# Optimization experiments

Hardware: AMD Instinct MI355X
Metric: run time of the kernel (lower is better)

## Reference

```python
import jax, jax.numpy as jnp
import numpy as np

B = 8192
N_SUP = 4
N_EXH = 4
N_OUTER = 50      # solver default; torch loop breaks early on tol/stall, replicated via done mask
N_INNER = 15
TOL = 1e-3
DESIGN_PRESSURE = 500.0
DESIGN_FLOW = 2.0
MAX_PRESSURE = 800.0
MOTOR_EFF = 0.9


def setup_inputs() -> dict:
    key = jax.random.key(0)
    k1, k2, k3 = jax.random.split(key, 3)
    fan_speed = 0.5 + 0.5 * jax.random.uniform(k1, (B,), dtype=jnp.float32)
    supply_damper_pos = 0.2 + 0.8 * jax.random.uniform(k2, (B, N_SUP), dtype=jnp.float32)
    exhaust_damper_pos = 0.2 + 0.8 * jax.random.uniform(k3, (B, N_EXH), dtype=jnp.float32)
    # FanModel.__init__ parameter init
    max_flow = DESIGN_FLOW * 1.3
    a_init = MAX_PRESSURE * 1000.0
    c_init = -MAX_PRESSURE * 1000.0 / max_flow ** 2
    b_init = (DESIGN_PRESSURE - a_init - c_init * DESIGN_FLOW ** 2) / DESIGN_FLOW
    fan_a = jnp.asarray(a_init / 1000.0, jnp.float32)
    fan_b = jnp.asarray(b_init, jnp.float32)
    fan_c = jnp.asarray(c_init, jnp.float32)
    # BranchModel / DamperModel parameter init (vectorized over branches)
    def branch_params(n):
        return (jnp.full((n,), np.log(50.0), jnp.float32),            # log_R_duct
                jnp.full((n,), 5.0, jnp.float32),                     # R_linear
                jnp.full((n,), np.log(10.0), jnp.float32),            # damper log_R_open
                jnp.full((n,), np.log(100000.0 / 10.0), jnp.float32)) # damper k
    slr, srl, sdo, sdk = branch_params(N_SUP)
    elr, erl, edo, edk = branch_params(N_EXH)
    return {
        'fan_speed': fan_speed,
        'supply_damper_pos': supply_damper_pos,
        'exhaust_damper_pos': exhaust_damper_pos,
        'fan_a': fan_a, 'fan_b': fan_b, 'fan_c': fan_c,
        'sup_log_R_duct': slr, 'sup_R_linear': srl, 'sup_damp_log_R_open': sdo, 'sup_damp_k': sdk,
        'exh_log_R_duct': elr, 'exh_R_linear': erl, 'exh_damp_log_R_open': edo, 'exh_damp_k': edk,
    }


def _branch_dp(flow, pos, log_R_duct, R_linear, damp_log_R_open, damp_k):
    # flow, pos: [B, n]; params: [n]; flow_exponent == 2.0
    aq = jnp.abs(flow)
    dp_duct = jnp.exp(log_R_duct) * aq ** 2 + jnp.abs(R_linear) * aq
    R_damp = jnp.exp(damp_log_R_open) * jnp.exp(damp_k * (1.0 - pos))
    return dp_duct + R_damp * aq ** 2


def _distribute(total_flow, pos, bp):
    n = pos.shape[1]
    flows = jnp.broadcast_to(total_flow[:, None] / n, pos.shape)
    for _ in range(N_INNER):
        p = _branch_dp(flows, pos, *bp)
        target = p.mean(axis=1, keepdims=True)
        R_eq = p / (flows ** 2 + 1e-6)
        new = jnp.sqrt(jnp.clip(target / (R_eq + 1e-6), 0.0, None))
        flows = new * total_flow[:, None] / (new.sum(axis=1, keepdims=True) + 1e-6)
    return flows, _branch_dp(flows, pos, *bp)


def _fan_pressure(flow, speed, a, b, c):
    fn = flow / (speed + 1e-6)
    pd = a * 1000.0 + b * fn + c * fn ** 2
    return jnp.maximum(pd * speed ** 2, 0.0)


def _forward(fan_speed, supply_damper_pos, exhaust_damper_pos, fan_a, fan_b, fan_c,
             sup_bp, exh_bp):
    def system_pressure(flow):
        _, sp = _distribute(flow, supply_damper_pos, sup_bp)
        _, ep = _distribute(flow, exhaust_damper_pos, exh_bp)
        return sp[:, 0] + ep[:, 0]

    flow_scale = DESIGN_FLOW / (DESIGN_PRESSURE + 1e-6)

    def step(carry, i):
        flow, prev_err, stall, done = carry
        res = _fan_pressure(flow, fan_speed, fan_a, fan_b, fan_c) - system_pressure(flow)
        err = jnp.max(jnp.abs(res))
        stalled = jnp.abs(err - prev_err) < 1e-6
        stall = jnp.where(stalled, stall + 1, 0)
        done = done | (err < TOL) | (stall > 10)
        alpha = jnp.maximum(0.5 * 0.95 ** i, 0.05)
        flow_new = jnp.clip(flow + alpha * res * flow_scale, 0.01, DESIGN_FLOW * 1.5)
        flow = jnp.where(done, flow, flow_new)
        prev_err = jnp.where(done, prev_err, err)
        return (flow, prev_err, stall, done), None

    init = (fan_speed * DESIGN_FLOW,
            jnp.asarray(jnp.inf, jnp.float32),
            jnp.asarray(0, jnp.int32),
            jnp.asarray(False))
    (flow, _, _, _), _ = jax.lax.scan(step, init, jnp.arange(N_OUTER, dtype=jnp.float32))

    flow = jnp.maximum(flow, 0.0)
    fan_p = _fan_pressure(flow, fan_speed, fan_a, fan_b, fan_c)
    sys_p = system_pressure(flow)
    # FanModel.get_power
    fr = flow / (DESIGN_FLOW + 1e-6)
    pr = fan_p / (DESIGN_PRESSURE + 1e-6)
    eta = jnp.clip(0.65 * (1.0 - 0.3 * (fr - 1.0) ** 2 - 0.2 * (pr - 1.0) ** 2), 0.3, 0.75)
    power = flow * fan_p / (eta * MOTOR_EFF + 1e-6)
    sf, sp = _distribute(flow, supply_damper_pos, sup_bp)
    ef, ep = _distribute(flow, exhaust_damper_pos, exh_bp)
    # pack dict outputs into one [B, 4 + 2*N_SUP + 2*N_EXH] array
    return jnp.concatenate([flow[:, None], fan_p[:, None], sys_p[:, None], power[:, None],
                            sf, sp, ef, ep], axis=1)


def reference(fan_speed, supply_damper_pos, exhaust_damper_pos, fan_a, fan_b, fan_c,
              sup_log_R_duct, sup_R_linear, sup_damp_log_R_open, sup_damp_k,
              exh_log_R_duct, exh_R_linear, exh_damp_log_R_open, exh_damp_k):
    sup_bp = (sup_log_R_duct, sup_R_linear, sup_damp_log_R_open, sup_damp_k)
    exh_bp = (exh_log_R_duct, exh_R_linear, exh_damp_log_R_open, exh_damp_k)
    return _forward(fan_speed, supply_damper_pos, exhaust_damper_pos,
                    fan_a, fan_b, fan_c, sup_bp, exh_bp)
```

## Files before the change

### kernel.cpp

```cpp
#include <hip/hip_runtime.h>
#include <math.h>

#define BATCH   8192
#define NOUTER  50
#define NINNER  15
#define NTHREADS (BATCH * 8)
#define NWAVES  (NTHREADS / 64)

__device__ __forceinline__ float fast_rcp(float x)  { return __builtin_amdgcn_rcpf(x); }
__device__ __forceinline__ float fast_sqrt(float x) { return __builtin_amdgcn_sqrtf(x); }

template <int CTRL>
__device__ __forceinline__ float dpp_movf(float x) {
    return __int_as_float(__builtin_amdgcn_update_dpp(
        0, __float_as_int(x), CTRL, 0xF, 0xF, true));
}
#define DPP_XOR1  0xB1
#define DPP_XOR2  0x4E
#define DPP_BQ0   0x00
#define DPP_ROR8  0x128
#define DPP_HMIR  0x141
#define DPP_BC15  0x142
#define DPP_BC31  0x143

__device__ __forceinline__ float distribute_lane(float total, float R2, float Rl,
                                                 float& pout) {
    float f = total * 0.25f;
#pragma unroll
    for (int it = 0; it < NINNER; ++it) {
        float p  = fmaf(R2, f * f, Rl * f);
        float t  = p + dpp_movf<DPP_XOR1>(p);
        t       += dpp_movf<DPP_XOR2>(t);
        float target = t * 0.25f;
        float q2e = fmaf(f, f, 1e-6f);
        float den = fmaf(q2e, 1e-6f, p);
        float ratio = target * q2e * fast_rcp(den);
        float nw = fast_sqrt(ratio);
        float s  = nw + dpp_movf<DPP_XOR1>(nw);
        s       += dpp_movf<DPP_XOR2>(s);
        f = nw * total * fast_rcp(s + 1e-6f);
    }
    pout = fmaf(R2, f * f, Rl * f);
    return f;
}

__device__ __forceinline__ float fan_pressure(float flow, float rspeed, float speed2,
                                              float a1000, float b, float c) {
    float fn = flow * rspeed;
    float pd = fmaf(c, fn * fn, fmaf(b, fn, a1000));
    return fmaxf(pd * speed2, 0.0f);
}

__device__ __forceinline__ float sys_from_p(float pfin) {
    float p0 = dpp_movf<DPP_BQ0>(pfin);
    return p0 + dpp_movf<DPP_HMIR>(p0);
}

struct LaneConsts {
    float R2, Rl;
    float speed, rspeed, speed2, a1000, b, c;
    int elem, lane, sub;
};

__device__ __forceinline__ LaneConsts setup_lane(
        const float* fan_speed,
        const float* sup_pos, const float* exh_pos,
        const float* pa, const float* pb, const float* pc,
        const float* slr, const float* srl, const float* sdo, const float* sdk,
        const float* elr, const float* erl, const float* edo, const float* edk) {
    LaneConsts L;
    int t   = blockIdx.x * blockDim.x + threadIdx.x;
    L.elem  = t >> 3;
    L.sub   = t & 7;
    int net = (L.sub >> 2) & 1;
    int j   = L.sub & 3;
    L.lane  = threadIdx.x & 63;

    const float* pos = net ? exh_pos : sup_pos;
    const float* lr  = net ? elr : slr;
    const float* rl  = net ? erl : srl;
    const float* dlo = net ? edo : sdo;
    const float* dk  = net ? edk : sdk;

    float Rduct = expf(lr[j]);
    float Rd    = expf(dlo[j]) * expf(dk[j] * (1.0f - pos[L.elem * 4 + j]));
    L.R2 = Rduct + Rd;
    L.Rl = fabsf(rl[j]);

    L.speed  = fan_speed[L.elem];
    L.rspeed = fast_rcp(L.speed + 1e-6f);
    L.speed2 = L.speed * L.speed;
    L.a1000  = pa[0] * 1000.0f;
    L.b      = pb[0];
    L.c      = pc[0];
    return L;
}

__global__ __launch_bounds__(256) void phase1(
        const float* __restrict__ fan_speed,
        const float* __restrict__ sup_pos, const float* __restrict__ exh_pos,
        const float* __restrict__ pa, const float* __restrict__ pb, const float* __restrict__ pc,
        const float* __restrict__ slr, const float* __restrict__ srl,
        const float* __restrict__ sdo, const float* __restrict__ sdk,
        const float* __restrict__ elr, const float* __restrict__ erl,
        const float* __restrict__ edo, const float* __restrict__ edk,
        float* __restrict__ slots, float* __restrict__ hist,
        float* __restrict__ stage, int use_hist) {
    LaneConsts L = setup_lane(fan_speed, sup_pos, exh_pos, pa, pb, pc,
                              slr, srl, sdo, sdk, elr, erl, edo, edk);
    int t = blockIdx.x * blockDim.x + threadIdx.x;
    int wave = t >> 6;
    const float flow_scale = 2.0f / (500.0f + 1e-6f);
    float flow = L.speed * 2.0f;
    float alpha_base = 0.5f;

#pragma unroll 1
    for (int i = 0; i < NOUTER; ++i) {
        float pfin;
        (void)distribute_lane(flow, L.R2, L.Rl, pfin);
        float sys  = sys_from_p(pfin);
        float res  = fan_pressure(flow, L.rspeed, L.speed2, L.a1000, L.b, L.c) - sys;
        float ares = fabsf(res);

        if (stage) {
            float m = fmaxf(ares, dpp_movf<DPP_ROR8>(ares));
            m = fmaxf(m, dpp_movf<DPP_BC15>(m));
            m = fmaxf(m, dpp_movf<DPP_BC31>(m));
            if (L.lane == 63)
                stage[i * NWAVES + wave] = m;
        } else {
            float m = ares;
            m = fmaxf(m, dpp_movf<DPP_ROR8>(m));
            m = fmaxf(m, __shfl_xor(m, 16));
            m = fmaxf(m, __shfl_xor(m, 32));
            if (L.lane == 0)
                atomicMax((int*)&slots[i], __float_as_int(m));
        }

        float alpha = fmaxf(alpha_base, 0.05f);
        alpha_base *= 0.95f;
        float fnew = fmaf(alpha * res, flow_scale, flow);
        flow = fminf(fmaxf(fnew, 0.01f), 3.0f);
        if (use_hist && L.sub == 0) hist[(size_t)i * BATCH + L.elem] = flow;
    }
}

__global__ __launch_bounds__(1024) void phase1b(const float* __restrict__ stage,
                                                int* __restrict__ kout) {
    __shared__ float sl[NOUTER];
    int lane = threadIdx.x & 63;
    int wv   = threadIdx.x >> 6;
#pragma unroll 1
    for (int i = wv; i < NOUTER; i += 16) {
        const float4* src = (const float4*)(stage + (size_t)i * NWAVES);
        float m = 0.0f;
#pragma unroll
        for (int q = 0; q < 4; ++q) {
            float4 v = src[lane + 64 * q];
            m = fmaxf(m, fmaxf(fmaxf(v.x, v.y), fmaxf(v.z, v.w)));
        }
#pragma unroll
        for (int off = 32; off; off >>= 1) m = fmaxf(m, __shfl_xor(m, off));
        if (lane == 0) sl[i] = m;
    }
    __syncthreads();
    if (threadIdx.x == 0) {
        float prev = INFINITY;
        int stall = 0, k = NOUTER;
        bool done = false;
#pragma unroll 1
        for (int i = 0; i < NOUTER; ++i) {
            float err = sl[i];
            bool stalled = fabsf(err - prev) < 1e-6f;
            stall = stalled ? stall + 1 : 0;
            done = done || (err < 1e-3f) || (stall > 10);
            if (done) { k = i; break; }
            prev = err;
        }
        *kout = k;
    }
}

template <bool USE_HIST>
__global__ __launch_bounds__(256) void phase3(
        const float* __restrict__ fan_speed,
        const float* __restrict__ sup_pos, const float* __restrict__ exh_pos,
        const float* __restrict__ pa, const float* __restrict__ pb, const float* __restrict__ pc,
        const float* __restrict__ slr, const float* __restrict__ srl,
        const float* __restrict__ sdo, const float* __restrict__ sdk,
        const float* __restrict__ elr, const float* __restrict__ erl,
        const float* __restrict__ edo, const float* __restrict__ edk,
        const float* __restrict__ slots, const int* __restrict__ kin, int use_k,
        const float* __restrict__ hist, float* __restrict__ out) {
    LaneConsts L = setup_lane(fan_speed, sup_pos, exh_pos, pa, pb, pc,
                              slr, srl, sdo, sdk, elr, erl, edo, edk);

    int k;
    if (use_k) {
        k = *kin;
    } else {
        float prev = INFINITY;
        int stall = 0; k = NOUTER;
        bool done = false;
#pragma unroll 1
        for (int i = 0; i < NOUTER; ++i) {
            float err = slots[i];
            bool stalled = fabsf(err - prev) < 1e-6f;
            stall = stalled ? stall + 1 : 0;
            done = done || (err < 1e-3f) || (stall > 10);
            if (done) { k = i; break; }
            prev = err;
        }
    }

    const float flow_scale = 2.0f / (500.0f + 1e-6f);
    float flow;
    if (USE_HIST) {
        flow = (k == 0) ? L.speed * 2.0f : hist[(size_t)(k - 1) * BATCH + L.elem];
    } else {
        flow = L.speed * 2.0f;
        float alpha_base = 0.5f;
#pragma unroll 1
        for (int i = 0; i < k; ++i) {
            float pfin;
            (void)distribute_lane(flow, L.R2, L.Rl, pfin);
            float sys = sys_from_p(pfin);
            float res = fan_pressure(flow, L.rspeed, L.speed2, L.a1000, L.b, L.c) - sys;
            float alpha = fmaxf(alpha_base, 0.05f);
            alpha_base *= 0.95f;
            float fnew = fmaf(alpha * res, flow_scale, flow);
            flow = fminf(fmaxf(fnew, 0.01f), 3.0f);
        }
    }

    flow = fmaxf(flow, 0.0f);
    float fanp = fan_pressure(flow, L.rspeed, L.speed2, L.a1000, L.b, L.c);

    float pfin;
    float ffin = distribute_lane(flow, L.R2, L.Rl, pfin);
    float sys  = sys_from_p(pfin);

    float fr  = flow * (1.0f / (2.0f + 1e-6f));
    float pr  = fanp * (1.0f / (500.0f + 1e-6f));
    float eta = 0.65f * (1.0f - 0.3f * (fr - 1.0f) * (fr - 1.0f)
                              - 0.2f * (pr - 1.0f) * (pr - 1.0f));
    eta = fminf(fmaxf(eta, 0.3f), 0.75f);
    float power = flow * fanp * fast_rcp(eta * 0.9f + 1e-6f);

    float* o = out + (size_t)L.elem * 20;
    if (L.sub == 0) {
        o[0] = flow; o[1] = fanp; o[2] = sys; o[3] = power;
    }
    int net = (L.sub >> 2) & 1;
    int j   = L.sub & 3;
    o[4 + net * 8 + j] = ffin;
    o[8 + net * 8 + j] = pfin;
}

extern "C" void kernel_launch(void* const* d_in, const int* in_sizes, int n_in,
                              void* d_out, int out_size, void* d_ws, size_t ws_size,
                              hipStream_t stream) {
    const float* fan_speed = (const float*)d_in[0];
    const float* sup_pos   = (const float*)d_in[1];
    const float* exh_pos   = (const float*)d_in[2];
    const float* pa        = (const float*)d_in[3];
    const float* pb        = (const float*)d_in[4];
    const float* pc        = (const float*)d_in[5];
    const float* slr       = (const float*)d_in[6];
    const float* srl       = (const float*)d_in[7];
    const float* sdo       = (const float*)d_in[8];
    const float* sdk       = (const float*)d_in[9];
    const float* elr       = (const float*)d_in[10];
    const float* erl       = (const float*)d_in[11];
    const float* edo       = (const float*)d_in[12];
    const float* edk       = (const float*)d_in[13];

    float* ws    = (float*)d_ws;
    float* slots = ws;
    int*   kptr  = (int*)(ws + 64);
    float* hist  = ws + 128;
    float* stage = ws + 128 + BATCH * NOUTER;

    size_t need_hist  = (size_t)(128 + BATCH * NOUTER) * sizeof(float);
    size_t need_stage = need_hist + (size_t)NOUTER * NWAVES * sizeof(float);
    bool use_hist  = ws_size >= need_hist;
    bool use_stage = ws_size >= need_stage;

    dim3 grid(NTHREADS / 256), block(256);

    phase1<<<grid, block, 0, stream>>>(fan_speed, sup_pos, exh_pos, pa, pb, pc,
                                       slr, srl, sdo, sdk, elr, erl, edo, edk,
                                       slots, hist, use_stage ? stage : nullptr,
                                       use_hist ? 1 : 0);
    if (use_stage)
        phase1b<<<dim3(1), dim3(1024), 0, stream>>>(stage, kptr);

    if (use_hist) {
        phase3<true><<<grid, block, 0, stream>>>(fan_speed, sup_pos, exh_pos, pa, pb, pc,
                                                 slr, srl, sdo, sdk, elr, erl, edo, edk,
                                                 slots, kptr, use_stage ? 1 : 0,
                                                 hist, (float*)d_out);
    } else {
        phase3<false><<<grid, block, 0, stream>>>(fan_speed, sup_pos, exh_pos, pa, pb, pc,
                                                  slr, srl, sdo, sdk, elr, erl, edo, edk,
                                                  slots, kptr, use_stage ? 1 : 0,
                                                  nullptr, (float*)d_out);
    }
}
```

Baseline: 134.0 us.

## Store per-element residuals and reduce them in a parallel multi-block pass

Phase1 no longer reduces the residual across its wave. Each element's lane 0 writes its absolute residual to a per-iteration staging array of BATCH floats. A new phase1b launches one block per outer iteration to compute the max, and a single-thread phase1c runs the convergence/stall scan. This removes DPP reductions from the solver loop and spreads the reduction across blocks, but it adds staging-buffer traffic, needs a larger workspace, and adds an extra kernel launch.

```diff
diff --git a/kernel.cpp b/kernel.cpp
--- a/kernel.cpp
+++ b/kernel.cpp
@@ -5,7 +5,6 @@
 #define NOUTER  50
 #define NINNER  15
 #define NTHREADS (BATCH * 8)
-#define NWAVES  (NTHREADS / 64)
 
 __device__ __forceinline__ float fast_rcp(float x)  { return __builtin_amdgcn_rcpf(x); }
 __device__ __forceinline__ float fast_sqrt(float x) { return __builtin_amdgcn_sqrtf(x); }
@@ -20,8 +19,6 @@
 #define DPP_BQ0   0x00
 #define DPP_ROR8  0x128
 #define DPP_HMIR  0x141
-#define DPP_BC15  0x142
-#define DPP_BC31  0x143
 
 __device__ __forceinline__ float distribute_lane(float total, float R2, float Rl,
                                                  float& pout) {
@@ -108,8 +105,6 @@
         float* __restrict__ stage, int use_hist) {
     LaneConsts L = setup_lane(fan_speed, sup_pos, exh_pos, pa, pb, pc,
                               slr, srl, sdo, sdk, elr, erl, edo, edk);
-    int t = blockIdx.x * blockDim.x + threadIdx.x;
-    int wave = t >> 6;
     const float flow_scale = 2.0f / (500.0f + 1e-6f);
     float flow = L.speed * 2.0f;
     float alpha_base = 0.5f;
@@ -123,11 +118,8 @@
         float ares = fabsf(res);
 
         if (stage) {
-            float m = fmaxf(ares, dpp_movf<DPP_ROR8>(ares));
-            m = fmaxf(m, dpp_movf<DPP_BC15>(m));
-            m = fmaxf(m, dpp_movf<DPP_BC31>(m));
-            if (L.lane == 63)
-                stage[i * NWAVES + wave] = m;
+            if (L.sub == 0)
+                stage[(size_t)i * BATCH + L.elem] = ares;
         } else {
             float m = ares;
             m = fmaxf(m, dpp_movf<DPP_ROR8>(m));
@@ -145,40 +137,38 @@
     }
 }
 
-__global__ __launch_bounds__(1024) void phase1b(const float* __restrict__ stage,
-                                                int* __restrict__ kout) {
-    __shared__ float sl[NOUTER];
-    int lane = threadIdx.x & 63;
-    int wv   = threadIdx.x >> 6;
+__global__ __launch_bounds__(256) void phase1b(const float* __restrict__ stage,
+                                               float* __restrict__ slots) {
+    const float4* src = (const float4*)(stage + (size_t)blockIdx.x * BATCH);
+    float m = 0.0f;
+#pragma unroll
+    for (int q = 0; q < 8; ++q) {
+        float4 v = src[threadIdx.x + 256 * q];
+        m = fmaxf(m, fmaxf(fmaxf(v.x, v.y), fmaxf(v.z, v.w)));
+    }
+#pragma unroll
+    for (int off = 32; off; off >>= 1) m = fmaxf(m, __shfl_xor(m, off));
+    __shared__ float red[4];
+    if ((threadIdx.x & 63) == 0) red[threadIdx.x >> 6] = m;
+    __syncthreads();
+    if (threadIdx.x == 0)
+        slots[blockIdx.x] = fmaxf(fmaxf(red[0], red[1]), fmaxf(red[2], red[3]));
+}
+
+__global__ void phase1c(const float* __restrict__ slots, int* __restrict__ kout) {
+    float prev = INFINITY;
+    int stall = 0, k = NOUTER;
+    bool done = false;
 #pragma unroll 1
-    for (int i = wv; i < NOUTER; i += 16) {
-        const float4* src = (const float4*)(stage + (size_t)i * NWAVES);
-        float m = 0.0f;
-#pragma unroll
-        for (int q = 0; q < 4; ++q) {
-            float4 v = src[lane + 64 * q];
-            m = fmaxf(m, fmaxf(fmaxf(v.x, v.y), fmaxf(v.z, v.w)));
-        }
-#pragma unroll
-        for (int off = 32; off; off >>= 1) m = fmaxf(m, __shfl_xor(m, off));
-        if (lane == 0) sl[i] = m;
-    }
-    __syncthreads();
-    if (threadIdx.x == 0) {
-        float prev = INFINITY;
-        int stall = 0, k = NOUTER;
-        bool done = false;
-#pragma unroll 1
-        for (int i = 0; i < NOUTER; ++i) {
-            float err = sl[i];
-            bool stalled = fabsf(err - prev) < 1e-6f;
-            stall = stalled ? stall + 1 : 0;
-            done = done || (err < 1e-3f) || (stall > 10);
-            if (done) { k = i; break; }
-            prev = err;
-        }
-        *kout = k;
-    }
+    for (int i = 0; i < NOUTER; ++i) {
+        float err = slots[i];
+        bool stalled = fabsf(err - prev) < 1e-6f;
+        stall = stalled ? stall + 1 : 0;
+        done = done || (err < 1e-3f) || (stall > 10);
+        if (done) { k = i; break; }
+        prev = err;
+    }
+    *kout = k;
 }
 
 template <bool USE_HIST>
@@ -282,7 +272,7 @@
     float* stage = ws + 128 + BATCH * NOUTER;
 
     size_t need_hist  = (size_t)(128 + BATCH * NOUTER) * sizeof(float);
-    size_t need_stage = need_hist + (size_t)NOUTER * NWAVES * sizeof(float);
+    size_t need_stage = need_hist + (size_t)BATCH * NOUTER * sizeof(float);
     bool use_hist  = ws_size >= need_hist;
     bool use_stage = ws_size >= need_stage;
 
@@ -292,8 +282,10 @@
                                        slr, srl, sdo, sdk, elr, erl, edo, edk,
                                        slots, hist, use_stage ? stage : nullptr,
                                        use_hist ? 1 : 0);
-    if (use_stage)
-        phase1b<<<dim3(1), dim3(1024), 0, stream>>>(stage, kptr);
+    if (use_stage) {
+        phase1b<<<dim3(NOUTER), dim3(256), 0, stream>>>(stage, slots);
+        phase1c<<<dim3(1), dim3(1), 0, stream>>>(slots, kptr);
+    }
 
     if (use_hist) {
         phase3<true><<<grid, block, 0, stream>>>(fan_speed, sup_pos, exh_pos, pa, pb, pc,
```

New measurement: 134.3 us. About the same (+0.2%).
